# Performance work log

Hardware: AMD Instinct MI355X
Metric: run time of the kernel (lower is better)

Reference implementation:

```python
import math
import jax, jax.numpy as jnp
import numpy as np

B, S, D = 8, 2048, 512
D_MODEL = 512

def setup_inputs() -> dict:
    key = jax.random.key(0)
    kq, kk, kv = jax.random.split(key, 3)
    return {
        "query": jax.random.normal(kq, (B, S, D), dtype=jnp.float32),
        "key":   jax.random.normal(kk, (B, S, D), dtype=jnp.float32),
        "value": jax.random.normal(kv, (B, S, D), dtype=jnp.float32),
    }

def reference(query, key, value):
    # scores: [B, S, S]
    scores = jnp.einsum("bqd,bkd->bqk", query, key) / math.sqrt(D_MODEL)
    k = max(1, int(scores.shape[-1] * 0.1))
    top_scores, top_idx = jax.lax.top_k(scores, k)  # [B, S, k]
    # scatter top-k scores into a zero matrix (non-topk entries stay 0,
    # and DO participate in the softmax, matching the torch code)
    b_idx = jnp.arange(scores.shape[0])[:, None, None]
    q_idx = jnp.arange(scores.shape[1])[None, :, None]
    sparse = jnp.zeros_like(scores).at[b_idx, q_idx, top_idx].set(top_scores)
    attn = jax.nn.softmax(sparse, axis=-1)
    return jnp.einsum("bqk,bkd->bqd", attn, value)
```

## Files before the change

### kernel.cpp

```cpp
#include <hip/hip_runtime.h>
#include <math.h>

#define B_ 8
#define S_ 2048
#define D_ 512
#define KTOP 204
#define QK_SCALE 0.044194173824159216f

typedef short bfrag8 __attribute__((ext_vector_type(8)));
typedef float facc4 __attribute__((ext_vector_type(4)));

__device__ __forceinline__ unsigned short f2bf(float f) {
  unsigned u = __float_as_uint(f);
  u += 0x7FFFu + ((u >> 16) & 1);
  return (unsigned short)(u >> 16);
}

__device__ __forceinline__ unsigned fkey(float f) {
  unsigned b = __float_as_uint(f);
  return (b & 0x80000000u) ? ~b : (b | 0x80000000u);
}
__device__ __forceinline__ float keyfloat(unsigned k) {
  unsigned b = (k & 0x80000000u) ? (k & 0x7FFFFFFFu) : ~k;
  return __uint_as_float(b);
}

__device__ __forceinline__ void load16(const unsigned short* g, unsigned short* l) {
  __builtin_amdgcn_global_load_lds(
      (const __attribute__((address_space(1))) void*)g,
      (__attribute__((address_space(3))) void*)l, 16, 0, 0);
}

__global__ __launch_bounds__(256) void cvt_qk(const float* __restrict__ Q,
                                              const float* __restrict__ K,
                                              unsigned short* __restrict__ Qb,
                                              unsigned short* __restrict__ Kb) {
  const float* in = blockIdx.y ? K : Q;
  unsigned short* out = blockIdx.y ? Kb : Qb;
  int i = (blockIdx.x * 256 + threadIdx.x) * 4;
  float4 v = *(const float4*)(in + i);
  ushort4 o;
  o.x = f2bf(v.x); o.y = f2bf(v.y); o.z = f2bf(v.z); o.w = f2bf(v.w);
  *(ushort4*)(out + i) = o;
}

__global__ __launch_bounds__(256) void transpose_v(const float* __restrict__ V,
                                                   unsigned short* __restrict__ VT) {
  __shared__ float tile[32][33];
  int b = blockIdx.z;
  int d0 = blockIdx.x * 32, k0 = blockIdx.y * 32;
  const float* Vb = V + (size_t)b * S_ * D_;
  unsigned short* VTb = VT + (size_t)b * D_ * S_;
  int c = threadIdx.x & 31, r = threadIdx.x >> 5;
#pragma unroll
  for (int rr = 0; rr < 32; rr += 8)
    tile[r + rr][c] = Vb[(size_t)(k0 + r + rr) * D_ + d0 + c];
  __syncthreads();
#pragma unroll
  for (int rr = 0; rr < 32; rr += 8)
    VTb[(size_t)(d0 + r + rr) * S_ + k0 + c] = f2bf(tile[c][r + rr]);
}

__global__ __launch_bounds__(256) void gemm_qk(
    const unsigned short* __restrict__ A, int lda, long long astr,
    const unsigned short* __restrict__ Bm, int ldb, long long bstr,
    float* __restrict__ C, int ldc, long long cstr,
    int kdim, float scale) {
  const unsigned j = blockIdx.x + 16u * blockIdx.y + 256u * blockIdx.z;
  const unsigned bz = j & 7u;
  const unsigned q = j >> 3;
  const unsigned by = q & 15u;
  const unsigned bx = q >> 4;

  __shared__ unsigned short smA[128 * 32];
  __shared__ unsigned short smB[128 * 32];
  const int tid = threadIdx.x;
  const int wave = tid >> 6, lane = tid & 63;
  const int quad = lane >> 4, l15 = lane & 15;
  const unsigned short* Ab = A + (long long)bz * astr + (size_t)(by * 128) * lda;
  const unsigned short* Bb = Bm + (long long)bz * bstr + (size_t)(bx * 128) * ldb;
  const int srow = tid >> 2;
  const int scol = (tid & 3) * 8;
  unsigned short* lA0 = smA + wave * 512;
  unsigned short* lA1 = smA + 2048 + wave * 512;
  unsigned short* lB0 = smB + wave * 512;
  unsigned short* lB1 = smB + 2048 + wave * 512;
  const int mrow = 64 * (wave >> 1);
  const int nrow = 64 * (wave & 1);

  facc4 acc[4][4];
  const facc4 fzero = {0.f, 0.f, 0.f, 0.f};
#pragma unroll
  for (int i = 0; i < 4; ++i)
#pragma unroll
    for (int j2 = 0; j2 < 4; ++j2) acc[i][j2] = fzero;

  for (int k0 = 0; k0 < kdim; k0 += 32) {
    __syncthreads();
    load16(Ab + (size_t)srow * lda + k0 + scol, lA0);
    load16(Ab + (size_t)(srow + 64) * lda + k0 + scol, lA1);
    load16(Bb + (size_t)srow * ldb + k0 + scol, lB0);
    load16(Bb + (size_t)(srow + 64) * ldb + k0 + scol, lB1);
    __syncthreads();
    bfrag8 af[4], bq[4];
#pragma unroll
    for (int i = 0; i < 4; ++i)
      af[i] = *(const bfrag8*)(smA + (mrow + 16 * i + l15) * 32 + quad * 8);
#pragma unroll
    for (int j2 = 0; j2 < 4; ++j2)
      bq[j2] = *(const bfrag8*)(smB + (nrow + 16 * j2 + l15) * 32 + quad * 8);
#pragma unroll
    for (int i = 0; i < 4; ++i)
#pragma unroll
      for (int j2 = 0; j2 < 4; ++j2)
        acc[i][j2] = __builtin_amdgcn_mfma_f32_16x16x32_bf16(af[i], bq[j2], acc[i][j2], 0, 0, 0);
  }

  float* Cb = C + (long long)bz * cstr;
  const int mg = by * 128 + mrow;
  const int ng = bx * 128 + nrow;
#pragma unroll
  for (int i = 0; i < 4; ++i)
#pragma unroll
    for (int j2 = 0; j2 < 4; ++j2)
#pragma unroll
      for (int r = 0; r < 4; ++r)
        Cb[(size_t)(mg + 16 * i + quad * 4 + r) * ldc + ng + 16 * j2 + l15] = acc[i][j2][r] * scale;
}

__global__ __launch_bounds__(256) void gemm_pv(
    const unsigned short* __restrict__ A, int lda, long long astr,
    const unsigned short* __restrict__ Bm, int ldb, long long bstr,
    float* __restrict__ C, int ldc, long long cstr,
    int kdim, float scale) {
  const unsigned j = blockIdx.x + 4u * blockIdx.y + 64u * blockIdx.z;
  const unsigned bz = j & 7u;
  const unsigned q = j >> 3;
  const unsigned bx = q & 3u;
  const unsigned by = q >> 2;

  __shared__ unsigned short smA[128 * 32];
  __shared__ unsigned short smB[128 * 32];
  const int tid = threadIdx.x;
  const int wave = tid >> 6, lane = tid & 63;
  const int quad = lane >> 4, l15 = lane & 15;
  const unsigned short* Ab = A + (long long)bz * astr + (size_t)(by * 128) * lda;
  const unsigned short* Bb = Bm + (long long)bz * bstr + (size_t)(bx * 128) * ldb;
  const int srow = tid >> 2;
  const int scol = (tid & 3) * 8;
  unsigned short* lA0 = smA + wave * 512;
  unsigned short* lA1 = smA + 2048 + wave * 512;
  unsigned short* lB0 = smB + wave * 512;
  unsigned short* lB1 = smB + 2048 + wave * 512;
  const int mrow = 64 * (wave >> 1);
  const int nrow = 64 * (wave & 1);

  facc4 acc[4][4];
  const facc4 fzero = {0.f, 0.f, 0.f, 0.f};
#pragma unroll
  for (int i = 0; i < 4; ++i)
#pragma unroll
    for (int j2 = 0; j2 < 4; ++j2) acc[i][j2] = fzero;

  for (int k0 = 0; k0 < kdim; k0 += 32) {
    __syncthreads();
    load16(Ab + (size_t)srow * lda + k0 + scol, lA0);
    load16(Ab + (size_t)(srow + 64) * lda + k0 + scol, lA1);
    load16(Bb + (size_t)srow * ldb + k0 + scol, lB0);
    load16(Bb + (size_t)(srow + 64) * ldb + k0 + scol, lB1);
    __syncthreads();
    bfrag8 af[4], bq[4];
#pragma unroll
    for (int i = 0; i < 4; ++i)
      af[i] = *(const bfrag8*)(smA + (mrow + 16 * i + l15) * 32 + quad * 8);
#pragma unroll
    for (int j2 = 0; j2 < 4; ++j2)
      bq[j2] = *(const bfrag8*)(smB + (nrow + 16 * j2 + l15) * 32 + quad * 8);
#pragma unroll
    for (int i = 0; i < 4; ++i)
#pragma unroll
      for (int j2 = 0; j2 < 4; ++j2)
        acc[i][j2] = __builtin_amdgcn_mfma_f32_16x16x32_bf16(af[i], bq[j2], acc[i][j2], 0, 0, 0);
  }

  float* Cb = C + (long long)bz * cstr;
  const int mg = by * 128 + mrow;
  const int ng = bx * 128 + nrow;
#pragma unroll
  for (int i = 0; i < 4; ++i)
#pragma unroll
    for (int j2 = 0; j2 < 4; ++j2)
#pragma unroll
      for (int r = 0; r < 4; ++r)
        Cb[(size_t)(mg + 16 * i + quad * 4 + r) * ldc + ng + 16 * j2 + l15] = acc[i][j2][r] * scale;
}

__device__ __forceinline__ unsigned sel256(const unsigned* bins, int lane,
                                           unsigned krem, unsigned* krem_out) {
  const uint4 b = *(const uint4*)(bins + lane * 4);
  const unsigned s = b.x + b.y + b.z + b.w;
  unsigned t = s;
#pragma unroll
  for (int off = 1; off < 64; off <<= 1) {
    unsigned u = (unsigned)__shfl_down((int)t, off);
    t += (lane + off < 64) ? u : 0u;
  }
  const unsigned texcl = t - s;
  const unsigned c3 = texcl + b.w;
  const unsigned c2 = c3 + b.z;
  const unsigned c1 = c2 + b.y;
  const unsigned c0 = c1 + b.x;
  unsigned pack = 0;
  if (c0 >= krem && c1 < krem)    pack = ((krem - c1) << 8) | (lane * 4 + 0);
  if (c1 >= krem && c2 < krem)    pack = ((krem - c2) << 8) | (lane * 4 + 1);
  if (c2 >= krem && c3 < krem)    pack = ((krem - c3) << 8) | (lane * 4 + 2);
  if (c3 >= krem && texcl < krem) pack = ((krem - texcl) << 8) | (lane * 4 + 3);
#pragma unroll
  for (int off = 1; off < 64; off <<= 1)
    pack |= (unsigned)__shfl_xor((int)pack, off);
  *krem_out = pack >> 8;
  return pack & 255u;
}

__global__ __launch_bounds__(256) void topk_softmax(float* __restrict__ scores) {
  __shared__ unsigned binsAll[4][256];
  const int tid = threadIdx.x;
  const int wave = tid >> 6, lane = tid & 63;
  const long long row = (long long)blockIdx.x * 4 + wave;
  float* srow = scores + row * 2048;
  unsigned* bins = binsAll[wave];

  unsigned k[32];
#pragma unroll
  for (int c = 0; c < 4; ++c) {
    float4 a = *(const float4*)(srow + c * 512 + lane * 8);
    float4 b = *(const float4*)(srow + c * 512 + lane * 8 + 4);
    k[c * 8 + 0] = fkey(a.x); k[c * 8 + 1] = fkey(a.y);
    k[c * 8 + 2] = fkey(a.z); k[c * 8 + 3] = fkey(a.w);
    k[c * 8 + 4] = fkey(b.x); k[c * 8 + 5] = fkey(b.y);
    k[c * 8 + 6] = fkey(b.z); k[c * 8 + 7] = fkey(b.w);
  }

  unsigned kmax = 0;
#pragma unroll
  for (int i = 0; i < 32; ++i) kmax = max(kmax, k[i]);
#pragma unroll
  for (int off = 1; off < 64; off <<= 1)
    kmax = max(kmax, (unsigned)__shfl_xor((int)kmax, off));
  const float m = fmaxf(keyfloat(kmax), 0.f);

  {
    uint4 z; z.x = 0; z.y = 0; z.z = 0; z.w = 0;
    *(uint4*)(bins + lane * 4) = z;
  }
#pragma unroll
  for (int i = 0; i < 32; ++i) {
    const int t = (int)(k[i] >> 16) - 0xBF00;
    if (t >= 1) atomicAdd(&bins[min(t, 255)], 1u);
  }
  unsigned krem;
  const unsigned d1 = sel256(bins, lane, KTOP, &krem);

  unsigned tkey;
  if (d1 >= 1u && d1 <= 254u) {
    const unsigned top16 = 0xBF00u + d1;
    { uint4 z; z.x = 0; z.y = 0; z.z = 0; z.w = 0; *(uint4*)(bins + lane * 4) = z; }
#pragma unroll
    for (int i = 0; i < 32; ++i)
      if ((k[i] >> 16) == top16) atomicAdd(&bins[(k[i] >> 8) & 255u], 1u);
    const unsigned b1 = sel256(bins, lane, krem, &krem);
    const unsigned top24 = (top16 << 8) | b1;
    { uint4 z; z.x = 0; z.y = 0; z.z = 0; z.w = 0; *(uint4*)(bins + lane * 4) = z; }
#pragma unroll
    for (int i = 0; i < 32; ++i)
      if ((k[i] >> 8) == top24) atomicAdd(&bins[k[i] & 255u], 1u);
    const unsigned b0 = sel256(bins, lane, krem, &krem);
    tkey = (top24 << 8) | b0;
  } else {
    krem = KTOP;
    unsigned prefix = 0, mmask = 0;
    for (int shift = 24; shift >= 0; shift -= 8) {
      { uint4 z; z.x = 0; z.y = 0; z.z = 0; z.w = 0; *(uint4*)(bins + lane * 4) = z; }
#pragma unroll
      for (int i = 0; i < 32; ++i)
        if ((k[i] & mmask) == prefix) atomicAdd(&bins[(k[i] >> shift) & 255u], 1u);
      const unsigned dig = sel256(bins, lane, krem, &krem);
      prefix |= dig << shift;
      mmask |= 0xFFu << shift;
    }
    tkey = prefix;
  }

  unsigned cut;
  {
    unsigned tiem = 0;
#pragma unroll
    for (int i = 0; i < 32; ++i)
      if (k[i] == tkey) tiem |= 1u << i;
    unsigned need = krem;
    for (;;) {
      unsigned myidx = 0xFFFFFFFFu;
      if (tiem) {
        int i = __ffs((int)tiem) - 1;
        myidx = ((unsigned)(i >> 3)) * 512u + (unsigned)lane * 8u + (unsigned)(i & 7);
      }
      unsigned minidx = myidx;
#pragma unroll
      for (int off = 1; off < 64; off <<= 1)
        minidx = min(minidx, (unsigned)__shfl_xor((int)minidx, off));
      if (--need == 0 || minidx == 0xFFFFFFFFu) { cut = minidx; break; }
      if (myidx == minidx) tiem &= tiem - 1;
    }
  }

  const float eqw = __expf(keyfloat(tkey) - m);
  const float base = __expf(-m);
  float zsum = 0.f;
#pragma unroll
  for (int i = 0; i < 32; ++i) {
    const unsigned key = k[i];
    const unsigned idx = ((unsigned)(i >> 3)) * 512u + (unsigned)lane * 8u + (unsigned)(i & 7);
    float w;
    if (key > tkey) w = __expf(keyfloat(key) - m);
    else w = (key == tkey && idx <= cut) ? eqw : base;
    zsum += w;
    k[i] = __float_as_uint(w);
  }
#pragma unroll
  for (int off = 1; off < 64; off <<= 1) zsum += __shfl_xor(zsum, off);
  const float invZ = 1.f / zsum;

  unsigned short* arow = (unsigned short*)scores + row * 4096;
#pragma unroll
  for (int c = 0; c < 4; ++c) {
    union { unsigned short u[8]; int4 v4; } pk;
#pragma unroll
    for (int j = 0; j < 8; ++j)
      pk.u[j] = f2bf(__uint_as_float(k[c * 8 + j]) * invZ);
    *(int4*)(arow + c * 512 + lane * 8) = pk.v4;
  }
}

extern "C" void kernel_launch(void* const* d_in, const int* in_sizes, int n_in,
                              void* d_out, int out_size, void* d_ws, size_t ws_size,
                              hipStream_t stream) {
  const float* Q = (const float*)d_in[0];
  const float* K = (const float*)d_in[1];
  const float* V = (const float*)d_in[2];
  float* out = (float*)d_out;
  char* ws = (char*)d_ws;
  unsigned short* Qb = (unsigned short*)(ws);
  unsigned short* Kb = (unsigned short*)(ws + ((size_t)16 << 20));
  unsigned short* VT = (unsigned short*)(ws + ((size_t)32 << 20));
  float* scores = (float*)(ws + ((size_t)48 << 20));

  const int nel = B_ * S_ * D_;
  cvt_qk<<<dim3(nel / 1024, 2), 256, 0, stream>>>(Q, K, Qb, Kb);
  transpose_v<<<dim3(D_ / 32, S_ / 32, B_), 256, 0, stream>>>(V, VT);
  gemm_qk<<<dim3(S_ / 128, S_ / 128, B_), 256, 0, stream>>>(
      Qb, D_, (long long)S_ * D_, Kb, D_, (long long)S_ * D_,
      scores, S_, (long long)S_ * S_, D_, QK_SCALE);
  topk_softmax<<<B_ * S_ / 4, 256, 0, stream>>>(scores);
  gemm_pv<<<dim3(D_ / 128, S_ / 128, B_), 256, 0, stream>>>(
      (const unsigned short*)scores, 4096, (long long)S_ * 4096,
      VT, S_, (long long)D_ * S_, out, D_, (long long)S_ * D_, S_, 1.0f);
}
```

Baseline: 281.5 us.

## Double-buffer shared-memory tiles in QK and PV GEMMs to overlap loads with MFMA

Both bf16 GEMM kernels now use two LDS buffers per operand and issue the global-to-LDS load for the next K-slab before running MFMAs on the current one. This halves the barriers per K step and is meant to hide global load latency behind matrix math. It doubles LDS use per block, which may lower occupancy, and it assumes kdim is a multiple of 64.

```diff
diff --git a/kernel.cpp b/kernel.cpp
--- a/kernel.cpp
+++ b/kernel.cpp
@@ -61,6 +61,34 @@
     VTb[(size_t)(d0 + r + rr) * S_ + k0 + c] = f2bf(tile[c][r + rr]);
 }
 
+
+__device__ __forceinline__ void stage4(const unsigned short* Ab, const unsigned short* Bb,
+                                       int lda, int ldb, int k0, int srow, int scol,
+                                       unsigned short* dA0, unsigned short* dA1,
+                                       unsigned short* dB0, unsigned short* dB1) {
+  load16(Ab + (size_t)srow * lda + k0 + scol, dA0);
+  load16(Ab + (size_t)(srow + 64) * lda + k0 + scol, dA1);
+  load16(Bb + (size_t)srow * ldb + k0 + scol, dB0);
+  load16(Bb + (size_t)(srow + 64) * ldb + k0 + scol, dB1);
+}
+
+__device__ __forceinline__ void mfma_step(const unsigned short* sA, const unsigned short* sB,
+                                          int mrow, int nrow, int l15, int quad,
+                                          facc4 (&acc)[4][4]) {
+  bfrag8 af[4], bq[4];
+#pragma unroll
+  for (int i = 0; i < 4; ++i)
+    af[i] = *(const bfrag8*)(sA + (mrow + 16 * i + l15) * 32 + quad * 8);
+#pragma unroll
+  for (int j2 = 0; j2 < 4; ++j2)
+    bq[j2] = *(const bfrag8*)(sB + (nrow + 16 * j2 + l15) * 32 + quad * 8);
+#pragma unroll
+  for (int i = 0; i < 4; ++i)
+#pragma unroll
+    for (int j2 = 0; j2 < 4; ++j2)
+      acc[i][j2] = __builtin_amdgcn_mfma_f32_16x16x32_bf16(af[i], bq[j2], acc[i][j2], 0, 0, 0);
+}
+
 __global__ __launch_bounds__(256) void gemm_qk(
     const unsigned short* __restrict__ A, int lda, long long astr,
     const unsigned short* __restrict__ Bm, int ldb, long long bstr,
@@ -72,8 +100,8 @@
   const unsigned by = q & 15u;
   const unsigned bx = q >> 4;
 
-  __shared__ unsigned short smA[128 * 32];
-  __shared__ unsigned short smB[128 * 32];
+  __shared__ unsigned short smA[2][128 * 32];
+  __shared__ unsigned short smB[2][128 * 32];
   const int tid = threadIdx.x;
   const int wave = tid >> 6, lane = tid & 63;
   const int quad = lane >> 4, l15 = lane & 15;
@@ -81,10 +109,8 @@
   const unsigned short* Bb = Bm + (long long)bz * bstr + (size_t)(bx * 128) * ldb;
   const int srow = tid >> 2;
   const int scol = (tid & 3) * 8;
-  unsigned short* lA0 = smA + wave * 512;
-  unsigned short* lA1 = smA + 2048 + wave * 512;
-  unsigned short* lB0 = smB + wave * 512;
-  unsigned short* lB1 = smB + 2048 + wave * 512;
+  const int so0 = wave * 512;
+  const int so1 = 2048 + wave * 512;
   const int mrow = 64 * (wave >> 1);
   const int nrow = 64 * (wave & 1);
 
@@ -95,25 +121,20 @@
 #pragma unroll
     for (int j2 = 0; j2 < 4; ++j2) acc[i][j2] = fzero;
 
-  for (int k0 = 0; k0 < kdim; k0 += 32) {
+  stage4(Ab, Bb, lda, ldb, 0, srow, scol,
+         smA[0] + so0, smA[0] + so1, smB[0] + so0, smB[0] + so1);
+  __syncthreads();
+
+  for (int k0 = 0; k0 < kdim; k0 += 64) {
+    stage4(Ab, Bb, lda, ldb, k0 + 32, srow, scol,
+           smA[1] + so0, smA[1] + so1, smB[1] + so0, smB[1] + so1);
+    mfma_step(smA[0], smB[0], mrow, nrow, l15, quad, acc);
     __syncthreads();
-    load16(Ab + (size_t)srow * lda + k0 + scol, lA0);
-    load16(Ab + (size_t)(srow + 64) * lda + k0 + scol, lA1);
-    load16(Bb + (size_t)srow * ldb + k0 + scol, lB0);
-    load16(Bb + (size_t)(srow + 64) * ldb + k0 + scol, lB1);
+    if (k0 + 64 < kdim)
+      stage4(Ab, Bb, lda, ldb, k0 + 64, srow, scol,
+             smA[0] + so0, smA[0] + so1, smB[0] + so0, smB[0] + so1);
+    mfma_step(smA[1], smB[1], mrow, nrow, l15, quad, acc);
     __syncthreads();
-    bfrag8 af[4], bq[4];
-#pragma unroll
-    for (int i = 0; i < 4; ++i)
-      af[i] = *(const bfrag8*)(smA + (mrow + 16 * i + l15) * 32 + quad * 8);
-#pragma unroll
-    for (int j2 = 0; j2 < 4; ++j2)
-      bq[j2] = *(const bfrag8*)(smB + (nrow + 16 * j2 + l15) * 32 + quad * 8);
-#pragma unroll
-    for (int i = 0; i < 4; ++i)
-#pragma unroll
-      for (int j2 = 0; j2 < 4; ++j2)
-        acc[i][j2] = __builtin_amdgcn_mfma_f32_16x16x32_bf16(af[i], bq[j2], acc[i][j2], 0, 0, 0);
   }
 
   float* Cb = C + (long long)bz * cstr;
@@ -139,8 +160,8 @@
   const unsigned bx = q & 3u;
   const unsigned by = q >> 2;
 
-  __shared__ unsigned short smA[128 * 32];
-  __shared__ unsigned short smB[128 * 32];
+  __shared__ unsigned short smA[2][128 * 32];
+  __shared__ unsigned short smB[2][128 * 32];
   const int tid = threadIdx.x;
   const int wave = tid >> 6, lane = tid & 63;
   const int quad = lane >> 4, l15 = lane & 15;
@@ -148,10 +169,8 @@
   const unsigned short* Bb = Bm + (long long)bz * bstr + (size_t)(bx * 128) * ldb;
   const int srow = tid >> 2;
   const int scol = (tid & 3) * 8;
-  unsigned short* lA0 = smA + wave * 512;
-  unsigned short* lA1 = smA + 2048 + wave * 512;
-  unsigned short* lB0 = smB + wave * 512;
-  unsigned short* lB1 = smB + 2048 + wave * 512;
+  const int so0 = wave * 512;
+  const int so1 = 2048 + wave * 512;
   const int mrow = 64 * (wave >> 1);
   const int nrow = 64 * (wave & 1);
 
@@ -162,25 +181,20 @@
 #pragma unroll
     for (int j2 = 0; j2 < 4; ++j2) acc[i][j2] = fzero;
 
-  for (int k0 = 0; k0 < kdim; k0 += 32) {
+  stage4(Ab, Bb, lda, ldb, 0, srow, scol,
+         smA[0] + so0, smA[0] + so1, smB[0] + so0, smB[0] + so1);
+  __syncthreads();
+
+  for (int k0 = 0; k0 < kdim; k0 += 64) {
+    stage4(Ab, Bb, lda, ldb, k0 + 32, srow, scol,
+           smA[1] + so0, smA[1] + so1, smB[1] + so0, smB[1] + so1);
+    mfma_step(smA[0], smB[0], mrow, nrow, l15, quad, acc);
     __syncthreads();
-    load16(Ab + (size_t)srow * lda + k0 + scol, lA0);
-    load16(Ab + (size_t)(srow + 64) * lda + k0 + scol, lA1);
-    load16(Bb + (size_t)srow * ldb + k0 + scol, lB0);
-    load16(Bb + (size_t)(srow + 64) * ldb + k0 + scol, lB1);
+    if (k0 + 64 < kdim)
+      stage4(Ab, Bb, lda, ldb, k0 + 64, srow, scol,
+             smA[0] + so0, smA[0] + so1, smB[0] + so0, smB[0] + so1);
+    mfma_step(smA[1], smB[1], mrow, nrow, l15, quad, acc);
     __syncthreads();
-    bfrag8 af[4], bq[4];
-#pragma unroll
-    for (int i = 0; i < 4; ++i)
-      af[i] = *(const bfrag8*)(smA + (mrow + 16 * i + l15) * 32 + quad * 8);
-#pragma unroll
-    for (int j2 = 0; j2 < 4; ++j2)
-      bq[j2] = *(const bfrag8*)(smB + (nrow + 16 * j2 + l15) * 32 + quad * 8);
-#pragma unroll
-    for (int i = 0; i < 4; ++i)
-#pragma unroll
-      for (int j2 = 0; j2 < 4; ++j2)
-        acc[i][j2] = __builtin_amdgcn_mfma_f32_16x16x32_bf16(af[i], bq[j2], acc[i][j2], 0, 0, 0);
   }
 
   float* Cb = C + (long long)bz * cstr;
```

New measurement: 286.0 us. No clear change (+1.6%).

## Double-buffer GEMM LDS tiles with 64-wide K steps and XOR swizzle

Applied to the files above, without the earlier changes.

Both GEMM kernels (QK and PV) now stage 64-wide K slices into two LDS buffers, loading the next slice while the MFMAs consume the current one. This halves the barriers per K element and lets global-to-LDS traffic overlap with compute. An XOR swizzle on the column slot is meant to avoid LDS bank conflicts on fragment reads. LDS use rises fourfold per block, which may reduce occupancy, and the loop assumes kdim is a multiple of 128.

```diff
diff --git a/kernel.cpp b/kernel.cpp
--- a/kernel.cpp
+++ b/kernel.cpp
@@ -61,6 +61,40 @@
     VTb[(size_t)(d0 + r + rr) * S_ + k0 + c] = f2bf(tile[c][r + rr]);
 }
 
+
+__device__ __forceinline__ void stage64(const unsigned short* M, int ld, int k0,
+                                        int tid, unsigned short* dst) {
+  const int wave = tid >> 6;
+  const int row = tid >> 3;
+  const int col = ((tid & 7) ^ (row & 7)) * 8;
+  unsigned short* wdst = dst + wave * 512;
+  const unsigned short* src = M + (size_t)row * ld + k0 + col;
+#pragma unroll
+  for (int s = 0; s < 4; ++s)
+    load16(src + (size_t)(s * 32) * ld, wdst + s * 2048);
+}
+
+__device__ __forceinline__ void mfma_step64(const unsigned short* sA, const unsigned short* sB,
+                                            int mrow, int nrow, int l15, int quad,
+                                            facc4 (&acc)[4][4]) {
+#pragma unroll
+  for (int c = 0; c < 2; ++c) {
+    const int slot = ((c * 4 + quad) ^ (l15 & 7)) * 8;
+    bfrag8 af[4], bq[4];
+#pragma unroll
+    for (int i = 0; i < 4; ++i)
+      af[i] = *(const bfrag8*)(sA + (mrow + 16 * i + l15) * 64 + slot);
+#pragma unroll
+    for (int j2 = 0; j2 < 4; ++j2)
+      bq[j2] = *(const bfrag8*)(sB + (nrow + 16 * j2 + l15) * 64 + slot);
+#pragma unroll
+    for (int i = 0; i < 4; ++i)
+#pragma unroll
+      for (int j2 = 0; j2 < 4; ++j2)
+        acc[i][j2] = __builtin_amdgcn_mfma_f32_16x16x32_bf16(af[i], bq[j2], acc[i][j2], 0, 0, 0);
+  }
+}
+
 __global__ __launch_bounds__(256) void gemm_qk(
     const unsigned short* __restrict__ A, int lda, long long astr,
     const unsigned short* __restrict__ Bm, int ldb, long long bstr,
@@ -72,19 +106,13 @@
   const unsigned by = q & 15u;
   const unsigned bx = q >> 4;
 
-  __shared__ unsigned short smA[128 * 32];
-  __shared__ unsigned short smB[128 * 32];
+  __shared__ unsigned short smA[2][128 * 64];
+  __shared__ unsigned short smB[2][128 * 64];
   const int tid = threadIdx.x;
   const int wave = tid >> 6, lane = tid & 63;
   const int quad = lane >> 4, l15 = lane & 15;
   const unsigned short* Ab = A + (long long)bz * astr + (size_t)(by * 128) * lda;
   const unsigned short* Bb = Bm + (long long)bz * bstr + (size_t)(bx * 128) * ldb;
-  const int srow = tid >> 2;
-  const int scol = (tid & 3) * 8;
-  unsigned short* lA0 = smA + wave * 512;
-  unsigned short* lA1 = smA + 2048 + wave * 512;
-  unsigned short* lB0 = smB + wave * 512;
-  unsigned short* lB1 = smB + 2048 + wave * 512;
   const int mrow = 64 * (wave >> 1);
   const int nrow = 64 * (wave & 1);
 
@@ -95,25 +123,21 @@
 #pragma unroll
     for (int j2 = 0; j2 < 4; ++j2) acc[i][j2] = fzero;
 
-  for (int k0 = 0; k0 < kdim; k0 += 32) {
+  stage64(Ab, lda, 0, tid, smA[0]);
+  stage64(Bb, ldb, 0, tid, smB[0]);
+  __syncthreads();
+
+  for (int k0 = 0; k0 < kdim; k0 += 128) {
+    stage64(Ab, lda, k0 + 64, tid, smA[1]);
+    stage64(Bb, ldb, k0 + 64, tid, smB[1]);
+    mfma_step64(smA[0], smB[0], mrow, nrow, l15, quad, acc);
     __syncthreads();
-    load16(Ab + (size_t)srow * lda + k0 + scol, lA0);
-    load16(Ab + (size_t)(srow + 64) * lda + k0 + scol, lA1);
-    load16(Bb + (size_t)srow * ldb + k0 + scol, lB0);
-    load16(Bb + (size_t)(srow + 64) * ldb + k0 + scol, lB1);
+    if (k0 + 128 < kdim) {
+      stage64(Ab, lda, k0 + 128, tid, smA[0]);
+      stage64(Bb, ldb, k0 + 128, tid, smB[0]);
+    }
+    mfma_step64(smA[1], smB[1], mrow, nrow, l15, quad, acc);
     __syncthreads();
-    bfrag8 af[4], bq[4];
-#pragma unroll
-    for (int i = 0; i < 4; ++i)
-      af[i] = *(const bfrag8*)(smA + (mrow + 16 * i + l15) * 32 + quad * 8);
-#pragma unroll
-    for (int j2 = 0; j2 < 4; ++j2)
-      bq[j2] = *(const bfrag8*)(smB + (nrow + 16 * j2 + l15) * 32 + quad * 8);
-#pragma unroll
-    for (int i = 0; i < 4; ++i)
-#pragma unroll
-      for (int j2 = 0; j2 < 4; ++j2)
-        acc[i][j2] = __builtin_amdgcn_mfma_f32_16x16x32_bf16(af[i], bq[j2], acc[i][j2], 0, 0, 0);
   }
 
   float* Cb = C + (long long)bz * cstr;
@@ -139,19 +163,13 @@
   const unsigned bx = q & 3u;
   const unsigned by = q >> 2;
 
-  __shared__ unsigned short smA[128 * 32];
-  __shared__ unsigned short smB[128 * 32];
+  __shared__ unsigned short smA[2][128 * 64];
+  __shared__ unsigned short smB[2][128 * 64];
   const int tid = threadIdx.x;
   const int wave = tid >> 6, lane = tid & 63;
   const int quad = lane >> 4, l15 = lane & 15;
   const unsigned short* Ab = A + (long long)bz * astr + (size_t)(by * 128) * lda;
   const unsigned short* Bb = Bm + (long long)bz * bstr + (size_t)(bx * 128) * ldb;
-  const int srow = tid >> 2;
-  const int scol = (tid & 3) * 8;
-  unsigned short* lA0 = smA + wave * 512;
-  unsigned short* lA1 = smA + 2048 + wave * 512;
-  unsigned short* lB0 = smB + wave * 512;
-  unsigned short* lB1 = smB + 2048 + wave * 512;
   const int mrow = 64 * (wave >> 1);
   const int nrow = 64 * (wave & 1);
 
@@ -162,25 +180,21 @@
 #pragma unroll
     for (int j2 = 0; j2 < 4; ++j2) acc[i][j2] = fzero;
 
-  for (int k0 = 0; k0 < kdim; k0 += 32) {
+  stage64(Ab, lda, 0, tid, smA[0]);
+  stage64(Bb, ldb, 0, tid, smB[0]);
+  __syncthreads();
+
+  for (int k0 = 0; k0 < kdim; k0 += 128) {
+    stage64(Ab, lda, k0 + 64, tid, smA[1]);
+    stage64(Bb, ldb, k0 + 64, tid, smB[1]);
+    mfma_step64(smA[0], smB[0], mrow, nrow, l15, quad, acc);
     __syncthreads();
-    load16(Ab + (size_t)srow * lda + k0 + scol, lA0);
-    load16(Ab + (size_t)(srow + 64) * lda + k0 + scol, lA1);
-    load16(Bb + (size_t)srow * ldb + k0 + scol, lB0);
-    load16(Bb + (size_t)(srow + 64) * ldb + k0 + scol, lB1);
+    if (k0 + 128 < kdim) {
+      stage64(Ab, lda, k0 + 128, tid, smA[0]);
+      stage64(Bb, ldb, k0 + 128, tid, smB[0]);
+    }
+    mfma_step64(smA[1], smB[1], mrow, nrow, l15, quad, acc);
     __syncthreads();
-    bfrag8 af[4], bq[4];
-#pragma unroll
-    for (int i = 0; i < 4; ++i)
-      af[i] = *(const bfrag8*)(smA + (mrow + 16 * i + l15) * 32 + quad * 8);
-#pragma unroll
-    for (int j2 = 0; j2 < 4; ++j2)
-      bq[j2] = *(const bfrag8*)(smB + (nrow + 16 * j2 + l15) * 32 + quad * 8);
-#pragma unroll
-    for (int i = 0; i < 4; ++i)
-#pragma unroll
-      for (int j2 = 0; j2 < 4; ++j2)
-        acc[i][j2] = __builtin_amdgcn_mfma_f32_16x16x32_bf16(af[i], bq[j2], acc[i][j2], 0, 0, 0);
   }
 
   float* Cb = C + (long long)bz * cstr;
```

After: 268.2 us, median of 2. 4.7% less time.
